# Performance work log

Measured on AMD Instinct MI355X. Metric: run time of the kernel, lower is better.

## Reference

```python
import jax, jax.numpy as jnp
import numpy as np

N_AGT, N_CTX, E, D, NC = 100000, 10000, 1000000, 128, 2


def _gn(x, w, b, eps=1e-5):
    # GroupNorm(num_groups=1) on (N, C): normalize over channels, affine.
    m = jnp.mean(x, axis=-1, keepdims=True)
    v = jnp.mean((x - m) ** 2, axis=-1, keepdims=True)
    return (x - m) * jax.lax.rsqrt(v + eps) * w + b


def setup_inputs() -> dict:
    key = jax.random.key(0)
    ks = jax.random.split(key, 16)
    s = 0.05  # weight scale
    return {
        "agts": jax.random.normal(ks[0], (N_AGT, D), jnp.float32),
        "ctx": jax.random.normal(ks[1], (N_CTX, D), jnp.float32),
        "agt_ctrs": jax.random.normal(ks[2], (N_AGT, NC), jnp.float32),
        "ctx_ctrs": jax.random.normal(ks[3], (N_CTX, NC), jnp.float32),
        "hi": jax.random.randint(ks[4], (E,), 0, N_AGT, jnp.int32),
        "wi": jax.random.randint(ks[5], (E,), 0, N_CTX, jnp.int32),
        "dist_w1": jax.random.normal(ks[6], (D, NC), jnp.float32) * s,
        "dist_b1": jnp.zeros((D,), jnp.float32),
        "dist_w2": jax.random.normal(ks[7], (D, D), jnp.float32) * s,
        "dist_gw": jnp.ones((D,), jnp.float32),
        "dist_gb": jnp.zeros((D,), jnp.float32),
        "q_w": jax.random.normal(ks[8], (D, D), jnp.float32) * s,
        "q_gw": jnp.ones((D,), jnp.float32),
        "q_gb": jnp.zeros((D,), jnp.float32),
        "ctx_w1": jax.random.normal(ks[9], (D, 3 * D), jnp.float32) * s,
        "ctx_gw": jnp.ones((D,), jnp.float32),
        "ctx_gb": jnp.zeros((D,), jnp.float32),
        "ctx_w2": jax.random.normal(ks[10], (D, D), jnp.float32) * s,
        "agt_w": jax.random.normal(ks[11], (D, D), jnp.float32) * s,
        "norm_gw": jnp.ones((D,), jnp.float32),
        "norm_gb": jnp.zeros((D,), jnp.float32),
        "lin_w": jax.random.normal(ks[12], (D, D), jnp.float32) * s,
        "lin_gw": jnp.ones((D,), jnp.float32),
        "lin_gb": jnp.zeros((D,), jnp.float32),
    }


def reference(agts, ctx, agt_ctrs, ctx_ctrs, hi, wi,
              dist_w1, dist_b1, dist_w2, dist_gw, dist_gb,
              q_w, q_gw, q_gb,
              ctx_w1, ctx_gw, ctx_gb, ctx_w2,
              agt_w, norm_gw, norm_gb,
              lin_w, lin_gw, lin_gb):
    res = agts
    # per-edge relative displacement: [E, 2]
    d = agt_ctrs[hi] - ctx_ctrs[wi]
    # dist MLP: Linear(2,128)+ReLU, Linear(128,128,nobias)+GN+ReLU
    d = jax.nn.relu(d @ dist_w1.T + dist_b1)
    d = jax.nn.relu(_gn(d @ dist_w2.T, dist_gw, dist_gb))
    # query: Linear(128,128,nobias)+GN+ReLU on gathered agents
    q = jax.nn.relu(_gn(agts[hi] @ q_w.T, q_gw, q_gb))
    # concat-MLP over edges: [E, 384] -> [E, 128]
    c = jnp.concatenate([d, q, ctx[wi]], axis=1)
    c = jax.nn.relu(_gn(c @ ctx_w1.T, ctx_gw, ctx_gb))
    c = c @ ctx_w2.T
    # agent transform + index_add scatter of edge messages
    a = agts @ agt_w.T
    a = a.at[hi].add(c)
    a = jax.nn.relu(_gn(a, norm_gw, norm_gb))
    a = _gn(a @ lin_w.T, lin_gw, lin_gb)  # Linear block with act=False
    a = jax.nn.relu(a + res)
    return a
```

## Files before the change

kernel.cpp:

```cpp
#include <hip/hip_runtime.h>
#include <stdint.h>


#define N_AGT 100000
#define N_CTX 10000
#define NE    1000000
#define D     128

typedef __attribute__((ext_vector_type(8))) __bf16 bf16x8;
typedef __attribute__((ext_vector_type(4))) float f32x4;
typedef __attribute__((ext_vector_type(4))) unsigned int uint32x4;
typedef __attribute__((ext_vector_type(8))) unsigned short ushort8;

__device__ __forceinline__ float bf_lo(uint32_t u){ return __uint_as_float(u << 16); }
__device__ __forceinline__ float bf_hi(uint32_t u){ return __uint_as_float(u & 0xFFFF0000u); }
__device__ __forceinline__ uint16_t f2bf(float f){
  uint32_t u = __float_as_uint(f);
  u += 0x7FFFu + ((u >> 16) & 1u);
  return (uint16_t)(u >> 16);
}
__device__ __forceinline__ float bf2f(uint16_t v){ return __uint_as_float(((uint32_t)v) << 16); }

__device__ __forceinline__ f32x4 mfma16(bf16x8 a, bf16x8 b, f32x4 c){
  return __builtin_amdgcn_mfma_f32_16x16x32_bf16(a, b, c, 0, 0, 0);
}


__device__ __forceinline__ void stage_wsz(char* dst, const float* __restrict__ W,
                                          int rs, int co, int tid){
  for (int idx = tid; idx < 128*16; idx += 512){
    const int row = idx >> 4, ch = idx & 15;
    const float4 f0 = *(const float4*)(W + (size_t)row*rs + co + ch*8);
    const float4 f1 = *(const float4*)(W + (size_t)row*rs + co + ch*8 + 4);
    ushort8 u;
    u[0]=f2bf(f0.x); u[1]=f2bf(f0.y); u[2]=f2bf(f0.z); u[3]=f2bf(f0.w);
    u[4]=f2bf(f1.x); u[5]=f2bf(f1.y); u[6]=f2bf(f1.z); u[7]=f2bf(f1.w);
    *(uint32x4*)(dst + row*256 + ((ch*16) ^ ((row&7)<<4))) = __builtin_bit_cast(uint32x4, u);
  }
}

__device__ __forceinline__ bf16x8 ldfrag(const char* base, int row, int cb){
  return __builtin_bit_cast(bf16x8,
      *(const uint32x4*)(base + row*256 + (cb ^ ((row&7)<<4))));
}

__device__ __forceinline__ void mm_stage(const char* xb, const char* wm, int wv,
                                         int llo, int lhi, f32x4 acc[3][2]){
  #pragma unroll
  for (int kt = 0; kt < 4; kt++){
    const int cb = kt*64 + lhi*16;
    const bf16x8 b0 = ldfrag(wm, wv*32 + llo,      cb);
    const bf16x8 b1 = ldfrag(wm, wv*32 + 16 + llo, cb);
    #pragma unroll
    for (int mt = 0; mt < 3; mt++){
      const bf16x8 a = ldfrag(xb, mt*16 + llo, cb);
      acc[mt][0] = mfma16(a, b0, acc[mt][0]);
      acc[mt][1] = mfma16(a, b1, acc[mt][1]);
    }
  }
}

__device__ __forceinline__ void scat_acc(char* xb, const f32x4 acc[3][2],
                                         int wv, int llo, int lhi){
  #pragma unroll
  for (int mt = 0; mt < 3; mt++)
    #pragma unroll
    for (int ntl = 0; ntl < 2; ntl++)
      #pragma unroll
      for (int r = 0; r < 4; r++){
        const int m = mt*16 + lhi*4 + r;
        const int n = wv*32 + ntl*16 + llo;
        *(uint16_t*)(xb + m*256 + ((n*2) ^ ((m&7)<<4))) = f2bf(acc[mt][ntl][r]);
      }
}

__device__ __forceinline__ void gn_rowpass(char* xb, const int rr[3], int llo,
                                           const float gw[8], const float gb[8]){
  #pragma unroll
  for (int i = 0; i < 3; i++){
    const int row = rr[i];
    char* p = xb + row*256 + ((llo*16) ^ ((row&7)<<4));
    ushort8 u = __builtin_bit_cast(ushort8, *(const uint32x4*)p);
    float f[8]; float s = 0.f, ss = 0.f;
    #pragma unroll
    for (int j = 0; j < 8; j++){ f[j] = bf2f(u[j]); s += f[j]; ss += f[j]*f[j]; }
    #pragma unroll
    for (int m = 1; m < 16; m <<= 1){ s += __shfl_xor(s, m); ss += __shfl_xor(ss, m); }
    const float mean = s*(1.f/128.f);
    const float var  = ss*(1.f/128.f) - mean*mean;
    const float rstd = rsqrtf(var + 1e-5f);
    #pragma unroll
    for (int j = 0; j < 8; j++){
      const float g = fmaxf((f[j]-mean)*rstd*gw[j] + gb[j], 0.f);
      u[j] = f2bf(g);
    }
    *(uint32x4*)p = __builtin_bit_cast(uint32x4, u);
  }
}

#define NITER ((NE + 95) / 96)

__global__ __launch_bounds__(512, 2) void k_edge_mfma(
    const float* __restrict__ agt_ctrs, const float* __restrict__ ctx_ctrs,
    const int* __restrict__ hi, const int* __restrict__ wi,
    const float* __restrict__ dist_w1, const float* __restrict__ dist_b1,
    const float* __restrict__ dist_gw, const float* __restrict__ dist_gb,
    const float* __restrict__ ctx_gw, const float* __restrict__ ctx_gb,
    const float* __restrict__ dist_w2, const float* __restrict__ ctx_w1,
    const float* __restrict__ ctx_w2,
    const uint16_t* __restrict__ QW, const uint16_t* __restrict__ CtxP,
    float* __restrict__ A0){
  extern __shared__ __align__(16) char smem[];
  const int tid  = threadIdx.x;
  const int wave = tid >> 6, lane = tid & 63;
  const int grp  = wave >> 2, wv = wave & 3;
  const int lhi  = lane >> 4, llo = lane & 15;

  stage_wsz(smem,         dist_w2, 128, 0, tid);
  stage_wsz(smem + 32768, ctx_w1,  384, 0, tid);
  stage_wsz(smem + 65536, ctx_w2,  128, 0, tid);

  char* xb = smem + 98304 + grp*12288;
  int*  hb = (int*)(smem + 122880) + grp*96;

  const int c0 = llo*8;
  float w1x[8], w1y[8], b1v[8], dgw[8], dgb[8], cgw[8], cgb[8];
  #pragma unroll
  for (int j = 0; j < 8; j++){
    w1x[j] = dist_w1[(c0+j)*2 + 0];
    w1y[j] = dist_w1[(c0+j)*2 + 1];
    b1v[j] = dist_b1[c0+j];
    dgw[j] = dist_gw[c0+j]; dgb[j] = dist_gb[c0+j];
    cgw[j] = ctx_gw[c0+j];  cgb[j] = ctx_gb[c0+j];
  }
  __syncthreads();

  for (int it = blockIdx.x; it < NITER; it += gridDim.x){
    const long ebase = (long)it*96 + grp*48;
    if (wv == 0 && lane < 48){
      const long e = ebase + lane;
      int h = 0, w = 0;
      if (e < NE){ h = hi[e]; w = wi[e]; }
      hb[lane] = h; hb[48 + lane] = w;
    }
    __syncthreads();
    int rr[3], rh[3], rw[3];
    ushort8 qg[3], cg[3];
    float2 acs[3], ccs[3];
    #pragma unroll
    for (int i = 0; i < 3; i++){
      rr[i] = wv*12 + i*4 + lhi;
      rh[i] = hb[rr[i]]; rw[i] = hb[48 + rr[i]];
      qg[i]  = *(const ushort8*)&QW  [(size_t)rh[i]*D + c0];
      cg[i]  = *(const ushort8*)&CtxP[(size_t)rw[i]*D + c0];
      acs[i] = *(const float2*)&agt_ctrs[(size_t)rh[i]*2];
      ccs[i] = *(const float2*)&ctx_ctrs[(size_t)rw[i]*2];
    }
    #pragma unroll
    for (int i = 0; i < 3; i++){
      const float dx = acs[i].x - ccs[i].x, dy = acs[i].y - ccs[i].y;
      ushort8 u;
      #pragma unroll
      for (int j = 0; j < 8; j++)
        u[j] = f2bf(fmaxf(fmaf(dx, w1x[j], fmaf(dy, w1y[j], b1v[j])), 0.f));
      *(uint32x4*)(xb + rr[i]*256 + ((llo*16) ^ ((rr[i]&7)<<4))) =
          __builtin_bit_cast(uint32x4, u);
    }
    __syncthreads();
    f32x4 acc1[3][2];
    #pragma unroll
    for (int mt = 0; mt < 3; mt++){ acc1[mt][0] = (f32x4)0.f; acc1[mt][1] = (f32x4)0.f; }
    mm_stage(xb, smem, wv, llo, lhi, acc1);
    __syncthreads();
    #pragma unroll
    for (int i = 0; i < 3; i++){
      ushort8 u;
      #pragma unroll
      for (int j = 0; j < 8; j++) u[j] = f2bf(bf2f(qg[i][j]) + bf2f(cg[i][j]));
      *(uint32x4*)(xb + rr[i]*256 + ((llo*16) ^ ((rr[i]&7)<<4))) =
          __builtin_bit_cast(uint32x4, u);
    }
    __syncthreads();
    f32x4 acc2[3][2];
    #pragma unroll
    for (int mt = 0; mt < 3; mt++)
      #pragma unroll
      for (int ntl = 0; ntl < 2; ntl++)
        #pragma unroll
        for (int r = 0; r < 4; r++){
          const int m = mt*16 + lhi*4 + r;
          const int n = wv*32 + ntl*16 + llo;
          acc2[mt][ntl][r] = bf2f(*(const uint16_t*)(xb + m*256 + ((n*2) ^ ((m&7)<<4))));
        }
    __syncthreads();
    scat_acc(xb, acc1, wv, llo, lhi);
    __syncthreads();
    gn_rowpass(xb, rr, llo, dgw, dgb);
    __syncthreads();
    mm_stage(xb, smem + 32768, wv, llo, lhi, acc2);
    __syncthreads();
    scat_acc(xb, acc2, wv, llo, lhi);
    __syncthreads();
    gn_rowpass(xb, rr, llo, cgw, cgb);
    __syncthreads();
    f32x4 acc3[3][2];
    #pragma unroll
    for (int mt = 0; mt < 3; mt++){ acc3[mt][0] = (f32x4)0.f; acc3[mt][1] = (f32x4)0.f; }
    mm_stage(xb, smem + 65536, wv, llo, lhi, acc3);
    #pragma unroll
    for (int mt = 0; mt < 3; mt++)
      #pragma unroll
      for (int ntl = 0; ntl < 2; ntl++)
        #pragma unroll
        for (int r = 0; r < 4; r++){
          const int m = mt*16 + lhi*4 + r;
          if (ebase + m < NE){
            const int n = wv*32 + ntl*16 + llo;
            atomicAdd(&A0[(size_t)hb[m]*D + n], acc3[mt][ntl][r]);
          }
        }
    __syncthreads();
  }
}

#define NITER_A ((N_AGT + 95) / 96)

__global__ __launch_bounds__(512, 2) void k_agent_pre_mfma(
    const float* __restrict__ agts, const float* __restrict__ q_w,
    const float* __restrict__ ctx_w1, const float* __restrict__ agt_w,
    const float* __restrict__ q_gw, const float* __restrict__ q_gb,
    uint16_t* __restrict__ QW, float* __restrict__ A0){
  extern __shared__ __align__(16) char smem[];
  const int tid  = threadIdx.x;
  const int wave = tid >> 6, lane = tid & 63;
  const int grp  = wave >> 2, wv = wave & 3;
  const int lhi  = lane >> 4, llo = lane & 15;

  stage_wsz(smem,         q_w,    128, 0,   tid);
  stage_wsz(smem + 32768, agt_w,  128, 0,   tid);
  stage_wsz(smem + 65536, ctx_w1, 384, 128, tid);

  char* xb = smem + 98304 + grp*12288;
  const int c0 = llo*8;
  float qgw[8], qgb[8];
  #pragma unroll
  for (int j = 0; j < 8; j++){ qgw[j] = q_gw[c0+j]; qgb[j] = q_gb[c0+j]; }
  __syncthreads();

  const int tg = tid & 255;
  int rr[3];
  #pragma unroll
  for (int i = 0; i < 3; i++) rr[i] = wv*12 + i*4 + lhi;

  for (int it = blockIdx.x; it < NITER_A; it += gridDim.x){
    const int rbase = it*96 + grp*48;
    for (int idx = tg; idx < 48*32; idx += 256){
      const int row = idx >> 5, c4 = idx & 31;
      int gr = rbase + row; if (gr >= N_AGT) gr = N_AGT - 1;
      const float4 f = *(const float4*)(agts + (size_t)gr*D + c4*4);
      const uint32_t lo = ((uint32_t)f2bf(f.y) << 16) | (uint32_t)f2bf(f.x);
      const uint32_t hi2 = ((uint32_t)f2bf(f.w) << 16) | (uint32_t)f2bf(f.z);
      *(uint2*)(xb + row*256 + ((c4*8) ^ ((row&7)<<4))) = make_uint2(lo, hi2);
    }
    __syncthreads();
    f32x4 acc[3][2];
    #pragma unroll
    for (int mt = 0; mt < 3; mt++){ acc[mt][0] = (f32x4)0.f; acc[mt][1] = (f32x4)0.f; }
    mm_stage(xb, smem + 32768, wv, llo, lhi, acc);
    #pragma unroll
    for (int mt = 0; mt < 3; mt++)
      #pragma unroll
      for (int ntl = 0; ntl < 2; ntl++)
        #pragma unroll
        for (int r = 0; r < 4; r++){
          const int m = mt*16 + lhi*4 + r;
          if (rbase + m < N_AGT){
            const int n = wv*32 + ntl*16 + llo;
            A0[(size_t)(rbase + m)*D + n] = acc[mt][ntl][r];
          }
        }
    #pragma unroll
    for (int mt = 0; mt < 3; mt++){ acc[mt][0] = (f32x4)0.f; acc[mt][1] = (f32x4)0.f; }
    mm_stage(xb, smem, wv, llo, lhi, acc);
    __syncthreads();
    scat_acc(xb, acc, wv, llo, lhi);
    __syncthreads();
    gn_rowpass(xb, rr, llo, qgw, qgb);
    __syncthreads();
    #pragma unroll
    for (int mt = 0; mt < 3; mt++){ acc[mt][0] = (f32x4)0.f; acc[mt][1] = (f32x4)0.f; }
    mm_stage(xb, smem + 65536, wv, llo, lhi, acc);
    __syncthreads();
    scat_acc(xb, acc, wv, llo, lhi);
    __syncthreads();
    #pragma unroll
    for (int i = 0; i < 3; i++){
      const int row = rr[i], gr = rbase + row;
      if (gr < N_AGT){
        const uint32x4 u = *(const uint32x4*)(xb + row*256 + ((llo*16) ^ ((row&7)<<4)));
        *(uint32x4*)(QW + (size_t)gr*D + c0) = u;
      }
    }
    __syncthreads();
  }
}

__global__ __launch_bounds__(512, 4) void k_post_mfma(
    float* __restrict__ A0, const float* __restrict__ agts,
    const float* __restrict__ lin_w,
    const float* __restrict__ norm_gw, const float* __restrict__ norm_gb,
    const float* __restrict__ lin_gw, const float* __restrict__ lin_gb){
  extern __shared__ __align__(16) char smem[];
  const int tid  = threadIdx.x;
  const int wave = tid >> 6, lane = tid & 63;
  const int grp  = wave >> 2, wv = wave & 3;
  const int lhi  = lane >> 4, llo = lane & 15;

  stage_wsz(smem, lin_w, 128, 0, tid);
  char* xb = smem + 32768 + grp*12288;
  const int c0 = llo*8;
  float ngw[8], ngb[8], lgw[8], lgb[8];
  #pragma unroll
  for (int j = 0; j < 8; j++){
    ngw[j] = norm_gw[c0+j]; ngb[j] = norm_gb[c0+j];
    lgw[j] = lin_gw[c0+j];  lgb[j] = lin_gb[c0+j];
  }
  __syncthreads();

  int rr[3];
  #pragma unroll
  for (int i = 0; i < 3; i++) rr[i] = wv*12 + i*4 + lhi;

  for (int it = blockIdx.x; it < NITER_A; it += gridDim.x){
    const int rbase = it*96 + grp*48;
    #pragma unroll
    for (int i = 0; i < 3; i++){
      const int row = rr[i];
      int gr = rbase + row; if (gr >= N_AGT) gr = N_AGT - 1;
      const float4 a0 = *(const float4*)(A0 + (size_t)gr*D + c0);
      const float4 a1 = *(const float4*)(A0 + (size_t)gr*D + c0 + 4);
      float f[8] = {a0.x,a0.y,a0.z,a0.w,a1.x,a1.y,a1.z,a1.w};
      float s = 0.f, ss = 0.f;
      #pragma unroll
      for (int j = 0; j < 8; j++){ s += f[j]; ss += f[j]*f[j]; }
      #pragma unroll
      for (int m = 1; m < 16; m <<= 1){ s += __shfl_xor(s, m); ss += __shfl_xor(ss, m); }
      const float mean = s*(1.f/128.f);
      const float var  = ss*(1.f/128.f) - mean*mean;
      const float rstd = rsqrtf(var + 1e-5f);
      ushort8 u;
      #pragma unroll
      for (int j = 0; j < 8; j++)
        u[j] = f2bf(fmaxf((f[j]-mean)*rstd*ngw[j] + ngb[j], 0.f));
      *(uint32x4*)(xb + row*256 + ((llo*16) ^ ((row&7)<<4))) =
          __builtin_bit_cast(uint32x4, u);
    }
    __syncthreads();
    f32x4 acc[3][2];
    #pragma unroll
    for (int mt = 0; mt < 3; mt++){ acc[mt][0] = (f32x4)0.f; acc[mt][1] = (f32x4)0.f; }
    mm_stage(xb, smem, wv, llo, lhi, acc);
    __syncthreads();
    scat_acc(xb, acc, wv, llo, lhi);
    __syncthreads();
    #pragma unroll
    for (int i = 0; i < 3; i++){
      const int row = rr[i];
      const char* p = xb + row*256 + ((llo*16) ^ ((row&7)<<4));
      const ushort8 u = __builtin_bit_cast(ushort8, *(const uint32x4*)p);
      float f[8]; float s = 0.f, ss = 0.f;
      #pragma unroll
      for (int j = 0; j < 8; j++){ f[j] = bf2f(u[j]); s += f[j]; ss += f[j]*f[j]; }
      #pragma unroll
      for (int m = 1; m < 16; m <<= 1){ s += __shfl_xor(s, m); ss += __shfl_xor(ss, m); }
      const float mean = s*(1.f/128.f);
      const float var  = ss*(1.f/128.f) - mean*mean;
      const float rstd = rsqrtf(var + 1e-5f);
      const int gr = rbase + row;
      if (gr < N_AGT){
        const float4 r0 = *(const float4*)(agts + (size_t)gr*D + c0);
        const float4 r1 = *(const float4*)(agts + (size_t)gr*D + c0 + 4);
        const float res[8] = {r0.x,r0.y,r0.z,r0.w,r1.x,r1.y,r1.z,r1.w};
        float4 o0, o1;
        float o[8];
        #pragma unroll
        for (int j = 0; j < 8; j++)
          o[j] = fmaxf((f[j]-mean)*rstd*lgw[j] + lgb[j] + res[j], 0.f);
        o0.x=o[0]; o0.y=o[1]; o0.z=o[2]; o0.w=o[3];
        o1.x=o[4]; o1.y=o[5]; o1.z=o[6]; o1.w=o[7];
        *(float4*)(A0 + (size_t)gr*D + c0)     = o0;
        *(float4*)(A0 + (size_t)gr*D + c0 + 4) = o1;
      }
    }
    __syncthreads();
  }
}

__device__ __forceinline__ void stage_w4(uint32_t* wp, const float* __restrict__ W,
                                         int rs, int co, int tid, int nthr){
  for (int idx = tid; idx < 32*128; idx += nthr){
    int p2 = idx & 31, o = idx >> 5;
    const float4 f = *(const float4*)(W + (size_t)o*rs + co + p2*4);
    uint32_t lo = ((uint32_t)f2bf(f.y) << 16) | (uint32_t)f2bf(f.x);
    uint32_t hi = ((uint32_t)f2bf(f.w) << 16) | (uint32_t)f2bf(f.z);
    *(uint2*)&wp[(p2*128 + o)*2] = make_uint2(lo, hi);
  }
}

__device__ __forceinline__ float dot128(const uint32_t* wp, const float* xb, int o){
  float acc = 0.f;
  #pragma unroll 8
  for (int p2 = 0; p2 < 32; p2++){
    const uint2 w = *(const uint2*)&wp[(p2*128 + o)*2];
    const float4 x = *(const float4*)&xb[p2*4];
    acc += x.x*bf_lo(w.x) + x.y*bf_hi(w.x) + x.z*bf_lo(w.y) + x.w*bf_hi(w.y);
  }
  return acc;
}

__global__ __launch_bounds__(128) void k_ctx(const float* __restrict__ ctx,
                                             const float* __restrict__ ctx_w1,
                                             uint16_t* __restrict__ CtxP){
  __shared__ __align__(16) uint32_t wc[32*128*2];
  __shared__ __align__(16) float xbuf[128];
  const int tid = threadIdx.x;
  stage_w4(wc, ctx_w1, 384, 256, tid, 128);
  __syncthreads();
  for (int row = blockIdx.x; row < N_CTX; row += gridDim.x){
    __syncthreads();
    xbuf[tid] = ctx[(size_t)row*D + tid];
    __syncthreads();
    const float acc = dot128(wc, xbuf, tid);
    CtxP[(size_t)row*D + tid] = f2bf(acc);
  }
}

extern "C" void kernel_launch(void* const* d_in, const int* in_sizes, int n_in,
                              void* d_out, int out_size, void* d_ws, size_t ws_size,
                              hipStream_t stream){
  const float* agts     = (const float*)d_in[0];
  const float* ctx      = (const float*)d_in[1];
  const float* agt_ctrs = (const float*)d_in[2];
  const float* ctx_ctrs = (const float*)d_in[3];
  const int*   hi       = (const int*)d_in[4];
  const int*   wi       = (const int*)d_in[5];
  const float* dist_w1  = (const float*)d_in[6];
  const float* dist_b1  = (const float*)d_in[7];
  const float* dist_w2  = (const float*)d_in[8];
  const float* dist_gw  = (const float*)d_in[9];
  const float* dist_gb  = (const float*)d_in[10];
  const float* q_w      = (const float*)d_in[11];
  const float* q_gw     = (const float*)d_in[12];
  const float* q_gb     = (const float*)d_in[13];
  const float* ctx_w1   = (const float*)d_in[14];
  const float* ctx_gw   = (const float*)d_in[15];
  const float* ctx_gb   = (const float*)d_in[16];
  const float* ctx_w2   = (const float*)d_in[17];
  const float* agt_w    = (const float*)d_in[18];
  const float* norm_gw  = (const float*)d_in[19];
  const float* norm_gb  = (const float*)d_in[20];
  const float* lin_w    = (const float*)d_in[21];
  const float* lin_gw   = (const float*)d_in[22];
  const float* lin_gb   = (const float*)d_in[23];

  uint16_t* QW   = (uint16_t*)d_ws;
  uint16_t* CtxP = QW + (size_t)N_AGT * D;
  float*    A0   = (float*)d_out;

  const int EDGE_LDS = 123648;
  const int APRE_LDS = 122880;
  const int POST_LDS = 57344;
  hipFuncSetAttribute((const void*)k_edge_mfma,
                      hipFuncAttributeMaxDynamicSharedMemorySize, EDGE_LDS);
  hipFuncSetAttribute((const void*)k_agent_pre_mfma,
                      hipFuncAttributeMaxDynamicSharedMemorySize, APRE_LDS);
  hipFuncSetAttribute((const void*)k_post_mfma,
                      hipFuncAttributeMaxDynamicSharedMemorySize, POST_LDS);

  k_ctx<<<1024, 128, 0, stream>>>(ctx, ctx_w1, CtxP);
  k_agent_pre_mfma<<<256, 512, APRE_LDS, stream>>>(agts, q_w, ctx_w1, agt_w,
      q_gw, q_gb, QW, A0);
  k_edge_mfma<<<256, 512, EDGE_LDS, stream>>>(agt_ctrs, ctx_ctrs, hi, wi,
      dist_w1, dist_b1, dist_gw, dist_gb, ctx_gw, ctx_gb,
      dist_w2, ctx_w1, ctx_w2, QW, CtxP, A0);
  k_post_mfma<<<512, 512, POST_LDS, stream>>>(A0, agts, lin_w,
      norm_gw, norm_gb, lin_gw, lin_gb);
}
```

Measured before the change: 696.6 us.

## Double edge-kernel block to 1024 threads and fold q/ctx add into GroupNorm

The edge kernel now runs 1024-thread blocks with four 48-edge groups per iteration, sharing one copy of the staged weights in LDS. This is meant to raise resident waves per CU and hide gather latency better. The pre-projected query and context contributions are kept in registers and added to the row-layout result inside the GroupNorm pass. This replaces the earlier LDS round-trip that seeded the accumulator, and drops one extra LDS write/read and two barriers per iteration. In exchange, LDS use grows and register pressure rises under the new launch bounds.

```diff
diff --git a/kernel.cpp b/kernel.cpp
--- a/kernel.cpp
+++ b/kernel.cpp
@@ -27,8 +27,8 @@
 
 
 __device__ __forceinline__ void stage_wsz(char* dst, const float* __restrict__ W,
-                                          int rs, int co, int tid){
-  for (int idx = tid; idx < 128*16; idx += 512){
+                                          int rs, int co, int tid, int nthr){
+  for (int idx = tid; idx < 128*16; idx += nthr){
     const int row = idx >> 4, ch = idx & 15;
     const float4 f0 = *(const float4*)(W + (size_t)row*rs + co + ch*8);
     const float4 f1 = *(const float4*)(W + (size_t)row*rs + co + ch*8 + 4);
@@ -98,9 +98,38 @@
   }
 }
 
-#define NITER ((NE + 95) / 96)
-
-__global__ __launch_bounds__(512, 2) void k_edge_mfma(
+__device__ __forceinline__ void gn_rowpass_add(char* xb, const int rr[3], int llo,
+                                               const float gw[8], const float gb[8],
+                                               const ushort8 qs[3]){
+  #pragma unroll
+  for (int i = 0; i < 3; i++){
+    const int row = rr[i];
+    char* p = xb + row*256 + ((llo*16) ^ ((row&7)<<4));
+    ushort8 u = __builtin_bit_cast(ushort8, *(const uint32x4*)p);
+    float f[8]; float s = 0.f, ss = 0.f;
+    #pragma unroll
+    for (int j = 0; j < 8; j++){
+      f[j] = bf2f(u[j]) + bf2f(qs[i][j]);
+      s += f[j]; ss += f[j]*f[j];
+    }
+    #pragma unroll
+    for (int m = 1; m < 16; m <<= 1){ s += __shfl_xor(s, m); ss += __shfl_xor(ss, m); }
+    const float mean = s*(1.f/128.f);
+    const float var  = ss*(1.f/128.f) - mean*mean;
+    const float rstd = rsqrtf(var + 1e-5f);
+    #pragma unroll
+    for (int j = 0; j < 8; j++){
+      const float g = fmaxf((f[j]-mean)*rstd*gw[j] + gb[j], 0.f);
+      u[j] = f2bf(g);
+    }
+    *(uint32x4*)p = __builtin_bit_cast(uint32x4, u);
+  }
+}
+
+#define GE      192
+#define NITER_E ((NE + GE - 1) / GE)
+
+__global__ __launch_bounds__(1024, 4) void k_edge_mfma(
     const float* __restrict__ agt_ctrs, const float* __restrict__ ctx_ctrs,
     const int* __restrict__ hi, const int* __restrict__ wi,
     const float* __restrict__ dist_w1, const float* __restrict__ dist_b1,
@@ -116,12 +145,12 @@
   const int grp  = wave >> 2, wv = wave & 3;
   const int lhi  = lane >> 4, llo = lane & 15;
 
-  stage_wsz(smem,         dist_w2, 128, 0, tid);
-  stage_wsz(smem + 32768, ctx_w1,  384, 0, tid);
-  stage_wsz(smem + 65536, ctx_w2,  128, 0, tid);
+  stage_wsz(smem,         dist_w2, 128, 0, tid, 1024);
+  stage_wsz(smem + 32768, ctx_w1,  384, 0, tid, 1024);
+  stage_wsz(smem + 65536, ctx_w2,  128, 0, tid, 1024);
 
   char* xb = smem + 98304 + grp*12288;
-  int*  hb = (int*)(smem + 122880) + grp*96;
+  int*  hb = (int*)(smem + 147456) + grp*96;
 
   const int c0 = llo*8;
   float w1x[8], w1y[8], b1v[8], dgw[8], dgb[8], cgw[8], cgb[8];
@@ -135,8 +164,12 @@
   }
   __syncthreads();
 
-  for (int it = blockIdx.x; it < NITER; it += gridDim.x){
-    const long ebase = (long)it*96 + grp*48;
+  int rr[3];
+  #pragma unroll
+  for (int i = 0; i < 3; i++) rr[i] = wv*12 + i*4 + lhi;
+
+  for (long it = blockIdx.x; it < NITER_E; it += gridDim.x){
+    const long ebase = it*GE + grp*48;
     if (wv == 0 && lane < 48){
       const long e = ebase + lane;
       int h = 0, w = 0;
@@ -144,27 +177,36 @@
       hb[lane] = h; hb[48 + lane] = w;
     }
     __syncthreads();
-    int rr[3], rh[3], rw[3];
-    ushort8 qg[3], cg[3];
+    int rh[3], rw[3];
+    ushort8 qs[3];
     float2 acs[3], ccs[3];
-    #pragma unroll
-    for (int i = 0; i < 3; i++){
-      rr[i] = wv*12 + i*4 + lhi;
-      rh[i] = hb[rr[i]]; rw[i] = hb[48 + rr[i]];
-      qg[i]  = *(const ushort8*)&QW  [(size_t)rh[i]*D + c0];
-      cg[i]  = *(const ushort8*)&CtxP[(size_t)rw[i]*D + c0];
-      acs[i] = *(const float2*)&agt_ctrs[(size_t)rh[i]*2];
-      ccs[i] = *(const float2*)&ctx_ctrs[(size_t)rw[i]*2];
-    }
-    #pragma unroll
-    for (int i = 0; i < 3; i++){
-      const float dx = acs[i].x - ccs[i].x, dy = acs[i].y - ccs[i].y;
-      ushort8 u;
-      #pragma unroll
-      for (int j = 0; j < 8; j++)
-        u[j] = f2bf(fmaxf(fmaf(dx, w1x[j], fmaf(dy, w1y[j], b1v[j])), 0.f));
-      *(uint32x4*)(xb + rr[i]*256 + ((llo*16) ^ ((rr[i]&7)<<4))) =
-          __builtin_bit_cast(uint32x4, u);
+    {
+      ushort8 qg[3], cg[3];
+      #pragma unroll
+      for (int i = 0; i < 3; i++){
+        rh[i] = hb[rr[i]]; rw[i] = hb[48 + rr[i]];
+        qg[i]  = *(const ushort8*)&QW  [(size_t)rh[i]*D + c0];
+        cg[i]  = *(const ushort8*)&CtxP[(size_t)rw[i]*D + c0];
+        acs[i] = *(const float2*)&agt_ctrs[(size_t)rh[i]*2];
+        ccs[i] = *(const float2*)&ctx_ctrs[(size_t)rw[i]*2];
+      }
+      #pragma unroll
+      for (int i = 0; i < 3; i++){
+        const float dx = acs[i].x - ccs[i].x, dy = acs[i].y - ccs[i].y;
+        ushort8 u;
+        #pragma unroll
+        for (int j = 0; j < 8; j++)
+          u[j] = f2bf(fmaxf(fmaf(dx, w1x[j], fmaf(dy, w1y[j], b1v[j])), 0.f));
+        *(uint32x4*)(xb + rr[i]*256 + ((llo*16) ^ ((rr[i]&7)<<4))) =
+            __builtin_bit_cast(uint32x4, u);
+      }
+      #pragma unroll
+      for (int i = 0; i < 3; i++){
+        ushort8 u;
+        #pragma unroll
+        for (int j = 0; j < 8; j++) u[j] = f2bf(bf2f(qg[i][j]) + bf2f(cg[i][j]));
+        qs[i] = u;
+      }
     }
     __syncthreads();
     f32x4 acc1[3][2];
@@ -172,36 +214,18 @@
     for (int mt = 0; mt < 3; mt++){ acc1[mt][0] = (f32x4)0.f; acc1[mt][1] = (f32x4)0.f; }
     mm_stage(xb, smem, wv, llo, lhi, acc1);
     __syncthreads();
-    #pragma unroll
-    for (int i = 0; i < 3; i++){
-      ushort8 u;
-      #pragma unroll
-      for (int j = 0; j < 8; j++) u[j] = f2bf(bf2f(qg[i][j]) + bf2f(cg[i][j]));
-      *(uint32x4*)(xb + rr[i]*256 + ((llo*16) ^ ((rr[i]&7)<<4))) =
-          __builtin_bit_cast(uint32x4, u);
-    }
+    scat_acc(xb, acc1, wv, llo, lhi);
+    __syncthreads();
+    gn_rowpass(xb, rr, llo, dgw, dgb);
     __syncthreads();
     f32x4 acc2[3][2];
     #pragma unroll
-    for (int mt = 0; mt < 3; mt++)
-      #pragma unroll
-      for (int ntl = 0; ntl < 2; ntl++)
-        #pragma unroll
-        for (int r = 0; r < 4; r++){
-          const int m = mt*16 + lhi*4 + r;
-          const int n = wv*32 + ntl*16 + llo;
-          acc2[mt][ntl][r] = bf2f(*(const uint16_t*)(xb + m*256 + ((n*2) ^ ((m&7)<<4))));
-        }
-    __syncthreads();
-    scat_acc(xb, acc1, wv, llo, lhi);
-    __syncthreads();
-    gn_rowpass(xb, rr, llo, dgw, dgb);
-    __syncthreads();
+    for (int mt = 0; mt < 3; mt++){ acc2[mt][0] = (f32x4)0.f; acc2[mt][1] = (f32x4)0.f; }
     mm_stage(xb, smem + 32768, wv, llo, lhi, acc2);
     __syncthreads();
     scat_acc(xb, acc2, wv, llo, lhi);
     __syncthreads();
-    gn_rowpass(xb, rr, llo, cgw, cgb);
+    gn_rowpass_add(xb, rr, llo, cgw, cgb, qs);
     __syncthreads();
     f32x4 acc3[3][2];
     #pragma unroll
@@ -236,9 +260,9 @@
   const int grp  = wave >> 2, wv = wave & 3;
   const int lhi  = lane >> 4, llo = lane & 15;
 
-  stage_wsz(smem,         q_w,    128, 0,   tid);
-  stage_wsz(smem + 32768, agt_w,  128, 0,   tid);
-  stage_wsz(smem + 65536, ctx_w1, 384, 128, tid);
+  stage_wsz(smem,         q_w,    128, 0,   tid, 512);
+  stage_wsz(smem + 32768, agt_w,  128, 0,   tid, 512);
+  stage_wsz(smem + 65536, ctx_w1, 384, 128, tid, 512);
 
   char* xb = smem + 98304 + grp*12288;
   const int c0 = llo*8;
@@ -316,7 +340,7 @@
   const int grp  = wave >> 2, wv = wave & 3;
   const int lhi  = lane >> 4, llo = lane & 15;
 
-  stage_wsz(smem, lin_w, 128, 0, tid);
+  stage_wsz(smem, lin_w, 128, 0, tid, 512);
   char* xb = smem + 32768 + grp*12288;
   const int c0 = llo*8;
   float ngw[8], ngb[8], lgw[8], lgb[8];
@@ -381,8 +405,8 @@
         const float4 r0 = *(const float4*)(agts + (size_t)gr*D + c0);
         const float4 r1 = *(const float4*)(agts + (size_t)gr*D + c0 + 4);
         const float res[8] = {r0.x,r0.y,r0.z,r0.w,r1.x,r1.y,r1.z,r1.w};
+        float o[8];
         float4 o0, o1;
-        float o[8];
         #pragma unroll
         for (int j = 0; j < 8; j++)
           o[j] = fmaxf((f[j]-mean)*rstd*lgw[j] + lgb[j] + res[j], 0.f);
@@ -467,7 +491,7 @@
   uint16_t* CtxP = QW + (size_t)N_AGT * D;
   float*    A0   = (float*)d_out;
 
-  const int EDGE_LDS = 123648;
+  const int EDGE_LDS = 148992;
   const int APRE_LDS = 122880;
   const int POST_LDS = 57344;
   hipFuncSetAttribute((const void*)k_edge_mfma,
@@ -480,7 +504,7 @@
   k_ctx<<<1024, 128, 0, stream>>>(ctx, ctx_w1, CtxP);
   k_agent_pre_mfma<<<256, 512, APRE_LDS, stream>>>(agts, q_w, ctx_w1, agt_w,
       q_gw, q_gb, QW, A0);
-  k_edge_mfma<<<256, 512, EDGE_LDS, stream>>>(agt_ctrs, ctx_ctrs, hi, wi,
+  k_edge_mfma<<<256, 1024, EDGE_LDS, stream>>>(agt_ctrs, ctx_ctrs, hi, wi,
       dist_w1, dist_b1, dist_gw, dist_gb, ctx_gw, ctx_gb,
       dist_w2, ctx_w1, ctx_w2, QW, CtxP, A0);
   k_post_mfma<<<512, 512, POST_LDS, stream>>>(A0, agts, lin_w,
```

Result: slower. 855.9 us (+22.9%).
